# Optimization experiments

Measured on AMD Instinct MI355X. Metric: run time of the kernel, lower is better.

Reference implementation:

```python
import jax, jax.numpy as jnp
import numpy as np
from jax import lax


def setup_inputs() -> dict:
    key = jax.random.key(0)
    k1, k2 = jax.random.split(key)
    x = jax.random.normal(k1, (16, 256, 64, 64), dtype=jnp.float32)
    weight = jax.random.normal(k2, (1024, 256), dtype=jnp.float32)  # codebook (K, C)
    return {"x": x, "weight": weight}


def reference(x, weight):
    B, C, H, W = x.shape
    # (b c h w) -> (b h w) c
    xf = jnp.transpose(x, (0, 2, 3, 1)).reshape(-1, C)  # [N, C]
    d = (jnp.sum(xf * xf, axis=1, keepdims=True)
         + jnp.sum(weight * weight, axis=1)
         - 2.0 * (xf @ weight.T))
    indices = jnp.argmin(d, axis=1)  # [N], int
    z = weight[indices]  # [N, C] embedding lookup
    codebook_loss = jnp.mean((z - lax.stop_gradient(xf)) ** 2)
    commitment_loss = jnp.mean((xf - lax.stop_gradient(z)) ** 2)
    # straight-through estimator
    zq = xf + lax.stop_gradient(z - xf)
    zq = zq.reshape(B, H, W, C).transpose(0, 3, 1, 2)  # back to [B, C, H, W]
    sequence = indices.reshape(B, H, W)
    return zq, sequence, codebook_loss, commitment_loss
```

## Files before the change

### kernel.cpp

```cpp
#include <hip/hip_runtime.h>
#include <cfloat>
#include <climits>

#define B_   16
#define C_   256
#define K_   1024
#define HW_  4096
#define N_   (B_ * HW_)
#define CHW_ (C_ * HW_)

#define SEQ_OFF  16777216
#define LOSS_OFF (SEQ_OFF + N_)
#define WT_F    0
#define WN_F    262144
#define WNU_F   263168
#define WQ_F    264192
#define RLIST_F 395264
#define RCNT_F  526336
#define WMAX_F  526337

#define RL_CAP  131072
#define EPS_GAP 0.1f
#define XSCL    20.0f
#define XINV    0.05f
#define XOVF    6.3f

typedef int i32x4  __attribute__((ext_vector_type(4)));
typedef int i32x16 __attribute__((ext_vector_type(16)));

__device__ __forceinline__ int pack4b(int b0, int b1, int b2, int b3) {
    return (b0 & 0xFF) | ((b1 & 0xFF) << 8) | ((b2 & 0xFF) << 16) | ((b3 & 0xFF) << 24);
}

__global__ __launch_bounds__(256) void wmax_kernel(
    const float* __restrict__ w, unsigned* __restrict__ wmax_bits)
{
    const int tid = blockIdx.x * 256 + threadIdx.x;
    float mx = 0.f;
#pragma unroll
    for (int q = 0; q < 4; ++q) {
        const float4 v = reinterpret_cast<const float4*>(w)[tid * 4 + q];
        mx = fmaxf(mx, fmaxf(fmaxf(fabsf(v.x), fabsf(v.y)), fmaxf(fabsf(v.z), fabsf(v.w))));
    }
#pragma unroll
    for (int m = 1; m < 64; m <<= 1) mx = fmaxf(mx, __shfl_xor(mx, m, 64));
    if ((threadIdx.x & 63) == 0) atomicMax(wmax_bits, __float_as_uint(mx));
}

__global__ __launch_bounds__(256) void wprep_kernel(
    const float* __restrict__ w, const unsigned* __restrict__ wmax_bits,
    unsigned char* __restrict__ wq, float* __restrict__ w_t,
    float* __restrict__ wn, int* __restrict__ wnu)
{
    const int t = threadIdx.x;
    const int l = t & 63;
    const int k = blockIdx.x * 4 + (t >> 6);
    const float wmx = __uint_as_float(*wmax_bits);
    const float s   = 127.4f / wmx;
    const float d1  = wmx / 127.4f;
    const float sl  = s * 256.0f;

    const float4 v4 = *reinterpret_cast<const float4*>(w + (size_t)k * C_ + l * 4);
    float vv[4] = {v4.x, v4.y, v4.z, v4.w};
    float s2 = vv[0]*vv[0] + vv[1]*vv[1] + vv[2]*vv[2] + vv[3]*vv[3];
#pragma unroll
    for (int m = 1; m < 64; m <<= 1) s2 += __shfl_xor(s2, m, 64);

    const int chunk = k >> 5;
    const int col   = k & 31;
#pragma unroll
    for (int q = 0; q < 4; ++q) {
        const int c = l * 4 + q;
        const float v = vv[q];
        const int qh = (int)rintf(v * s);
        const float r = fmaf((float)qh, -d1, v);
        int ql = (int)rintf(r * sl);
        ql = max(-127, min(127, ql));
        const size_t off = (size_t)chunk * 16384 + (size_t)(c >> 5) * 1024
                         + (size_t)((c >> 4) & 1) * 512 + (size_t)col * 16 + (size_t)(c & 15);
        wq[off]        = (unsigned char)(qh & 0xFF);
        wq[off + 8192] = (unsigned char)(ql & 0xFF);
        w_t[(size_t)c * K_ + k] = v;
    }
    if (l == 0) {
        wn[k] = s2;
        wnu[k] = (int)rintf(s2 * (2560.0f / d1));
    }
}

__global__ __launch_bounds__(256) void argmin_i8_kernel(
    const float* __restrict__ x, const unsigned char* __restrict__ wq,
    const int* __restrict__ wnu, const unsigned* __restrict__ wmax_bits,
    float* __restrict__ seq, int* __restrict__ rlist, int* __restrict__ rcount)
{
    __shared__ __align__(16) int   wbuf[2][4096];
    __shared__ __align__(16) float xs[32][128];
    __shared__ int wnu_s[1024];

    const int t  = threadIdx.x;
    const int l  = t & 63;
    const int wv = t >> 6;
    const int col = l & 31;
    const int khalf = l >> 5;
    const int nb = blockIdx.x;
    const int b  = nb >> 5;
    const int hw0 = (nb & 31) << 7;
    const float* xb = x + (size_t)b * CHW_ + hw0;

#define STAGE32(ch, bufidx)                                                       \
    {                                                                             \
        _Pragma("unroll")                                                         \
        for (int rr = 0; rr < 4; ++rr) {                                          \
            const int sIdx = wv * 4 + rr;                                         \
            __builtin_amdgcn_global_load_lds(                                     \
                (const __attribute__((address_space(1))) void*)                   \
                    (wq + (size_t)(ch) * 16384 + sIdx * 1024 + l * 16),           \
                (__attribute__((address_space(3))) void*)                         \
                    (&wbuf[bufidx][sIdx * 256]), 16, 0, 0);                       \
        }                                                                         \
    }

    STAGE32(0, 0);

#pragma unroll
    for (int i = 0; i < 4; ++i) wnu_s[t + i * 256] = wnu[t + i * 256];

    i32x4 ah8[8], al8[8];
    float mx = 0.f;
    {
        const int row = wv * 32 + col;
#pragma unroll
        for (int cc = 0; cc < 8; ++cc) {
#pragma unroll
            for (int qq = 0; qq < 4; ++qq) {
                const int fi = qq * 256 + t;
                const int cl = fi >> 5;
                const int r4 = (fi & 31) << 2;
                const float4 v = *reinterpret_cast<const float4*>(
                    xb + (size_t)(cc * 32 + cl) * HW_ + r4);
                *reinterpret_cast<float4*>(&xs[cl][r4]) = v;
            }
            __syncthreads();
            int qh[16], ql[16];
#pragma unroll
            for (int j = 0; j < 16; ++j) {
                const float v = xs[khalf * 16 + j][row];
                mx = fmaxf(mx, fabsf(v));
                int h = (int)rintf(v * XSCL);
                h = max(-127, min(127, h));
                const float r = fmaf((float)h, -XINV, v);
                int lo = (int)rintf(r * (XSCL * 256.0f));
                lo = max(-127, min(127, lo));
                qh[j] = h; ql[j] = lo;
            }
            ah8[cc] = (i32x4){ pack4b(qh[0],qh[1],qh[2],qh[3]),   pack4b(qh[4],qh[5],qh[6],qh[7]),
                               pack4b(qh[8],qh[9],qh[10],qh[11]), pack4b(qh[12],qh[13],qh[14],qh[15]) };
            al8[cc] = (i32x4){ pack4b(ql[0],ql[1],ql[2],ql[3]),   pack4b(ql[4],ql[5],ql[6],ql[7]),
                               pack4b(ql[8],ql[9],ql[10],ql[11]), pack4b(ql[12],ql[13],ql[14],ql[15]) };
            __syncthreads();
        }
    }

    mx = fmaxf(mx, __shfl_xor(mx, 32, 64));
    if (khalf == 0 && mx > XOVF) {
        const int pos = atomicAdd(rcount, 1);
        if (pos < RL_CAP) rlist[pos] = b * HW_ + hw0 + wv * 32 + col;
    }

    const float wmx = __uint_as_float(*wmax_bits);
    const int eps_u = (int)(32614.4f / wmx);

    int m1p[16], m2p[16];
#pragma unroll
    for (int r = 0; r < 16; ++r) { m1p[r] = INT_MAX; m2p[r] = INT_MAX; }

#pragma unroll 1
    for (int ch = 0; ch < 32; ++ch) {
        const int cur = ch & 1;
        if (ch < 31) STAGE32(ch + 1, cur ^ 1);
        const int wnu_l = wnu_s[ch * 32 + col];

        i32x16 aH, aX;
#pragma unroll
        for (int r = 0; r < 16; ++r) { aH[r] = 0; aX[r] = 0; }

#pragma unroll
        for (int ks = 0; ks < 8; ++ks) {
            const i32x4 bh = *reinterpret_cast<const i32x4*>(&wbuf[cur][ks * 256 + (l << 2)]);
            const i32x4 bl = *reinterpret_cast<const i32x4*>(&wbuf[cur][2048 + ks * 256 + (l << 2)]);
            aH = __builtin_amdgcn_mfma_i32_32x32x32_i8(ah8[ks], bh, aH, 0, 0, 0);
            aX = __builtin_amdgcn_mfma_i32_32x32x32_i8(ah8[ks], bl, aX, 0, 0, 0);
            aX = __builtin_amdgcn_mfma_i32_32x32x32_i8(al8[ks], bh, aX, 0, 0, 0);
        }

#pragma unroll
        for (int r = 0; r < 16; ++r) {
            const int T  = (aH[r] << 8) + aX[r];
            const int D  = wnu_l - T;
            const int Dp = (D & ~31) | ch;
            m2p[r] = min(m2p[r], max(m1p[r], Dp));
            m1p[r] = min(m1p[r], Dp);
        }
        __syncthreads();
    }
#undef STAGE32

    int k1[16];
#pragma unroll
    for (int r = 0; r < 16; ++r) k1[r] = ((m1p[r] & 31) << 5) | col;
#pragma unroll
    for (int mask = 1; mask <= 16; mask <<= 1) {
#pragma unroll
        for (int r = 0; r < 16; ++r) {
            const int om1 = __shfl_xor(m1p[r], mask, 64);
            const int ok1 = __shfl_xor(k1[r],  mask, 64);
            const int om2 = __shfl_xor(m2p[r], mask, 64);
            const int nm2 = min(min(m2p[r], om2), max(m1p[r], om1));
            const bool lt = om1 < m1p[r] || (om1 == m1p[r] && ok1 < k1[r]);
            m1p[r] = lt ? om1 : m1p[r];
            k1[r]  = lt ? ok1 : k1[r];
            m2p[r] = nm2;
        }
    }

    if (col == 0) {
#pragma unroll
        for (int r = 0; r < 16; ++r) {
            const int row_local = (r & 3) + 8 * (r >> 2) + 4 * khalf;
            const int n = b * HW_ + hw0 + wv * 32 + row_local;
            seq[n] = (float)k1[r];
            if (m2p[r] - m1p[r] < eps_u) {
                const int pos = atomicAdd(rcount, 1);
                if (pos < RL_CAP) rlist[pos] = n;
            }
        }
    }
}

__global__ __launch_bounds__(256) void rescue_kernel(
    const float* __restrict__ x, const float* __restrict__ w_t,
    const float* __restrict__ wnorm, const int* __restrict__ rlist,
    const int* __restrict__ rcount, float* __restrict__ seq)
{
    __shared__ float xr[C_];
    __shared__ float bvs[4];
    __shared__ int   bis[4];
    const int t = threadIdx.x;
    const int cnt = min(*rcount, RL_CAP);
    for (int ii = blockIdx.x; ii < cnt; ii += gridDim.x) {
        const int n = rlist[ii];
        const int b = n >> 12, hw = n & 4095;
        xr[t] = x[(size_t)b * CHW_ + (size_t)t * HW_ + hw];
        __syncthreads();
        float best = FLT_MAX; int bidx = 0;
#pragma unroll
        for (int q = 0; q < 4; ++q) {
            const int k = t + q * 256;
            float acc = 0.f;
            for (int c = 0; c < C_; ++c) acc = fmaf(xr[c], w_t[(size_t)c * K_ + k], acc);
            const float d = wnorm[k] - 2.f * acc;
            if (d < best || (d == best && k < bidx)) { best = d; bidx = k; }
        }
#pragma unroll
        for (int mask = 1; mask < 64; mask <<= 1) {
            const float ov = __shfl_xor(best, mask, 64);
            const int   oi = __shfl_xor(bidx, mask, 64);
            if (ov < best || (ov == best && oi < bidx)) { best = ov; bidx = oi; }
        }
        if ((t & 63) == 0) { bvs[t >> 6] = best; bis[t >> 6] = bidx; }
        __syncthreads();
        if (t == 0) {
            float bv = bvs[0]; int bi = bis[0];
#pragma unroll
            for (int w2 = 1; w2 < 4; ++w2)
                if (bvs[w2] < bv || (bvs[w2] == bv && bis[w2] < bi)) { bv = bvs[w2]; bi = bis[w2]; }
            seq[n] = (float)bi;
        }
        __syncthreads();
    }
}

__global__ __launch_bounds__(256) void gather_kernel(
    const float* __restrict__ x, const float* __restrict__ w,
    const float* __restrict__ seqf, float* __restrict__ zq,
    double* __restrict__ loss_acc)
{
    __shared__ float ws[C_ * 64];
    const int t   = threadIdx.x;
    const int nb  = blockIdx.x;
    const int b   = nb >> 6;
    const int hw0 = (nb & 63) << 6;
    {
        const int j = t >> 2, q = t & 3;
        const int idx = (int)seqf[b * HW_ + hw0 + j];
        const float* wrow = w + (size_t)idx * C_ + q * 64;
#pragma unroll
        for (int m = 0; m < 16; ++m) {
            const float4 v = *reinterpret_cast<const float4*>(wrow + m * 4);
            const int c = q * 64 + m * 4;
            ws[(c + 0) * 64 + j] = v.x;
            ws[(c + 1) * 64 + j] = v.y;
            ws[(c + 2) * 64 + j] = v.z;
            ws[(c + 3) * 64 + j] = v.w;
        }
    }
    __syncthreads();
    const int r  = t & 63;
    const int cg = t >> 6;
    const float* xb = x  + (size_t)b * CHW_ + hw0;
    float*       zb = zq + (size_t)b * CHW_ + hw0;
    float lsum = 0.f;
#pragma unroll 4
    for (int cc = 0; cc < 64; ++cc) {
        const int c = cg * 64 + cc;
        const float xv = xb[(size_t)c * HW_ + r];
        const float d  = ws[c * 64 + r] - xv;
        zb[(size_t)c * HW_ + r] = xv + d;
        lsum += d * d;
    }
#pragma unroll
    for (int off = 32; off >= 1; off >>= 1) lsum += __shfl_down(lsum, off, 64);
    __syncthreads();
    if ((t & 63) == 0) ws[t >> 6] = lsum;
    __syncthreads();
    if (t == 0)
        atomicAdd(loss_acc, (double)(ws[0] + ws[1] + ws[2] + ws[3]));
}

__global__ void finalize_kernel(const double* __restrict__ acc, float* __restrict__ loss_out)
{
    const double s = *acc;
    const float m = (float)(s / (double)((size_t)N_ * C_));
    loss_out[0] = m;
    loss_out[1] = m;
}

extern "C" void kernel_launch(void* const* d_in, const int* in_sizes, int n_in,
                              void* d_out, int out_size, void* d_ws, size_t ws_size,
                              hipStream_t stream)
{
    (void)in_sizes; (void)n_in; (void)out_size; (void)d_ws; (void)ws_size;
    const float* x = (const float*)d_in[0];
    const float* w = (const float*)d_in[1];
    float* out = (float*)d_out;

    float*         w_t    = out + WT_F;
    float*         wn     = out + WN_F;
    int*           wnu    = (int*)(out + WNU_F);
    unsigned char* wq     = (unsigned char*)(out + WQ_F);
    int*           rlist  = (int*)(out + RLIST_F);
    int*           rcount = (int*)(out + RCNT_F);
    unsigned*      wmaxb  = (unsigned*)(out + WMAX_F);
    float*         seq    = out + SEQ_OFF;
    double*        loss_acc = (double*)(out + LOSS_OFF);

    hipMemsetAsync((void*)wmaxb, 0, 4, stream);
    hipMemsetAsync((void*)rcount, 0, 4, stream);
    wmax_kernel<<<64, 256, 0, stream>>>(w, wmaxb);
    wprep_kernel<<<256, 256, 0, stream>>>(w, wmaxb, wq, w_t, wn, wnu);
    argmin_i8_kernel<<<512, 256, 0, stream>>>(x, wq, wnu, wmaxb, seq, rlist, rcount);
    rescue_kernel<<<1024, 256, 0, stream>>>(x, w_t, wn, rlist, rcount, seq);
    hipMemsetAsync((char*)d_out + (size_t)LOSS_OFF * 4, 0, 8, stream);
    gather_kernel<<<1024, 256, 0, stream>>>(x, w, seq, out, loss_acc);
    finalize_kernel<<<1, 1, 0, stream>>>(loss_acc, out + LOSS_OFF);
}
```

Before: 201.6 us.

## Alias x staging buffer onto weight LDS and split MFMA accumulators

The 16KB x-staging buffer is removed and the x transpose staging now reuses weight buffer 0, with the first weight chunk prefetched into buffer 1 and the ping-pong order flipped to match. This cuts LDS per block, which may allow more resident blocks per CU. The int8 MFMA chain is also split across four independent accumulators instead of two, which shortens dependent MFMA chains at the cost of extra accumulator registers that could lower occupancy.

```diff
diff --git a/kernel.cpp b/kernel.cpp
--- a/kernel.cpp
+++ b/kernel.cpp
@@ -93,8 +93,7 @@
     const int* __restrict__ wnu, const unsigned* __restrict__ wmax_bits,
     float* __restrict__ seq, int* __restrict__ rlist, int* __restrict__ rcount)
 {
-    __shared__ __align__(16) int   wbuf[2][4096];
-    __shared__ __align__(16) float xs[32][128];
+    __shared__ __align__(16) int wbuf[2][4096];
     __shared__ int wnu_s[1024];
 
     const int t  = threadIdx.x;
@@ -120,7 +119,7 @@
         }                                                                         \
     }
 
-    STAGE32(0, 0);
+    STAGE32(0, 1);
 
 #pragma unroll
     for (int i = 0; i < 4; ++i) wnu_s[t + i * 256] = wnu[t + i * 256];
@@ -128,6 +127,7 @@
     i32x4 ah8[8], al8[8];
     float mx = 0.f;
     {
+        float* xs = reinterpret_cast<float*>(&wbuf[0][0]);
         const int row = wv * 32 + col;
 #pragma unroll
         for (int cc = 0; cc < 8; ++cc) {
@@ -138,13 +138,13 @@
                 const int r4 = (fi & 31) << 2;
                 const float4 v = *reinterpret_cast<const float4*>(
                     xb + (size_t)(cc * 32 + cl) * HW_ + r4);
-                *reinterpret_cast<float4*>(&xs[cl][r4]) = v;
+                *reinterpret_cast<float4*>(&xs[cl * 128 + r4]) = v;
             }
             __syncthreads();
             int qh[16], ql[16];
 #pragma unroll
             for (int j = 0; j < 16; ++j) {
-                const float v = xs[khalf * 16 + j][row];
+                const float v = xs[(khalf * 16 + j) * 128 + row];
                 mx = fmaxf(mx, fabsf(v));
                 int h = (int)rintf(v * XSCL);
                 h = max(-127, min(127, h));
@@ -176,26 +176,31 @@
 
 #pragma unroll 1
     for (int ch = 0; ch < 32; ++ch) {
-        const int cur = ch & 1;
+        const int cur = 1 ^ (ch & 1);
         if (ch < 31) STAGE32(ch + 1, cur ^ 1);
         const int wnu_l = wnu_s[ch * 32 + col];
 
-        i32x16 aH, aX;
-#pragma unroll
-        for (int r = 0; r < 16; ++r) { aH[r] = 0; aX[r] = 0; }
-
-#pragma unroll
-        for (int ks = 0; ks < 8; ++ks) {
-            const i32x4 bh = *reinterpret_cast<const i32x4*>(&wbuf[cur][ks * 256 + (l << 2)]);
-            const i32x4 bl = *reinterpret_cast<const i32x4*>(&wbuf[cur][2048 + ks * 256 + (l << 2)]);
-            aH = __builtin_amdgcn_mfma_i32_32x32x32_i8(ah8[ks], bh, aH, 0, 0, 0);
-            aX = __builtin_amdgcn_mfma_i32_32x32x32_i8(ah8[ks], bl, aX, 0, 0, 0);
-            aX = __builtin_amdgcn_mfma_i32_32x32x32_i8(al8[ks], bh, aX, 0, 0, 0);
+        i32x16 aH1, aH2, aX1, aX2;
+#pragma unroll
+        for (int r = 0; r < 16; ++r) { aH1[r] = 0; aH2[r] = 0; aX1[r] = 0; aX2[r] = 0; }
+
+#pragma unroll
+        for (int ks = 0; ks < 8; ks += 2) {
+            const i32x4 bh0 = *reinterpret_cast<const i32x4*>(&wbuf[cur][ks * 256 + (l << 2)]);
+            const i32x4 bl0 = *reinterpret_cast<const i32x4*>(&wbuf[cur][2048 + ks * 256 + (l << 2)]);
+            const i32x4 bh1 = *reinterpret_cast<const i32x4*>(&wbuf[cur][(ks + 1) * 256 + (l << 2)]);
+            const i32x4 bl1 = *reinterpret_cast<const i32x4*>(&wbuf[cur][2048 + (ks + 1) * 256 + (l << 2)]);
+            aH1 = __builtin_amdgcn_mfma_i32_32x32x32_i8(ah8[ks],     bh0, aH1, 0, 0, 0);
+            aH2 = __builtin_amdgcn_mfma_i32_32x32x32_i8(ah8[ks + 1], bh1, aH2, 0, 0, 0);
+            aX1 = __builtin_amdgcn_mfma_i32_32x32x32_i8(ah8[ks],     bl0, aX1, 0, 0, 0);
+            aX2 = __builtin_amdgcn_mfma_i32_32x32x32_i8(al8[ks],     bh0, aX2, 0, 0, 0);
+            aX1 = __builtin_amdgcn_mfma_i32_32x32x32_i8(ah8[ks + 1], bl1, aX1, 0, 0, 0);
+            aX2 = __builtin_amdgcn_mfma_i32_32x32x32_i8(al8[ks + 1], bh1, aX2, 0, 0, 0);
         }
 
 #pragma unroll
         for (int r = 0; r < 16; ++r) {
-            const int T  = (aH[r] << 8) + aX[r];
+            const int T  = ((aH1[r] + aH2[r]) << 8) + aX1[r] + aX2[r];
             const int D  = wnu_l - T;
             const int Dp = (D & ~31) | ch;
             m2p[r] = min(m2p[r], max(m1p[r], Dp));
```

Result: slower. 208.4 us (+3.3%).

## Drop LDS staging in argmin kernel; one wave per block reading codebook from global

Applied to the files above, without the earlier changes.

Restructures the int8 MFMA argmin kernel from 4-wave blocks that share a double-buffered LDS copy of the quantized codebook to single-wave blocks (2048 blocks of 64 threads). Each wave now loads its B operands straight from global memory into registers, and x is read per lane with strided scalar loads instead of coalesced float4 staging through LDS. This removes LDS traffic and all __syncthreads barriers, relying on L2/L1 for codebook reuse and on more resident waves to hide latency. In exchange, each wave fetches the full codebook itself, raising global and L2 traffic, and the x loads are less coalesced.

```diff
diff --git a/kernel.cpp b/kernel.cpp
--- a/kernel.cpp
+++ b/kernel.cpp
@@ -88,83 +88,45 @@
     }
 }
 
-__global__ __launch_bounds__(256) void argmin_i8_kernel(
+__global__ __launch_bounds__(64, 2) void argmin_i8_kernel(
     const float* __restrict__ x, const unsigned char* __restrict__ wq,
     const int* __restrict__ wnu, const unsigned* __restrict__ wmax_bits,
     float* __restrict__ seq, int* __restrict__ rlist, int* __restrict__ rcount)
 {
-    __shared__ __align__(16) int   wbuf[2][4096];
-    __shared__ __align__(16) float xs[32][128];
-    __shared__ int wnu_s[1024];
-
-    const int t  = threadIdx.x;
-    const int l  = t & 63;
-    const int wv = t >> 6;
+    const int l = threadIdx.x;
     const int col = l & 31;
     const int khalf = l >> 5;
     const int nb = blockIdx.x;
-    const int b  = nb >> 5;
-    const int hw0 = (nb & 31) << 7;
-    const float* xb = x + (size_t)b * CHW_ + hw0;
-
-#define STAGE32(ch, bufidx)                                                       \
-    {                                                                             \
-        _Pragma("unroll")                                                         \
-        for (int rr = 0; rr < 4; ++rr) {                                          \
-            const int sIdx = wv * 4 + rr;                                         \
-            __builtin_amdgcn_global_load_lds(                                     \
-                (const __attribute__((address_space(1))) void*)                   \
-                    (wq + (size_t)(ch) * 16384 + sIdx * 1024 + l * 16),           \
-                (__attribute__((address_space(3))) void*)                         \
-                    (&wbuf[bufidx][sIdx * 256]), 16, 0, 0);                       \
-        }                                                                         \
-    }
-
-    STAGE32(0, 0);
-
-#pragma unroll
-    for (int i = 0; i < 4; ++i) wnu_s[t + i * 256] = wnu[t + i * 256];
+    const int b  = nb >> 7;
+    const int hw0 = (nb & 127) << 5;
+    const float* xb = x + (size_t)b * CHW_ + hw0 + col;
 
     i32x4 ah8[8], al8[8];
     float mx = 0.f;
-    {
-        const int row = wv * 32 + col;
-#pragma unroll
-        for (int cc = 0; cc < 8; ++cc) {
-#pragma unroll
-            for (int qq = 0; qq < 4; ++qq) {
-                const int fi = qq * 256 + t;
-                const int cl = fi >> 5;
-                const int r4 = (fi & 31) << 2;
-                const float4 v = *reinterpret_cast<const float4*>(
-                    xb + (size_t)(cc * 32 + cl) * HW_ + r4);
-                *reinterpret_cast<float4*>(&xs[cl][r4]) = v;
-            }
-            __syncthreads();
-            int qh[16], ql[16];
-#pragma unroll
-            for (int j = 0; j < 16; ++j) {
-                const float v = xs[khalf * 16 + j][row];
-                mx = fmaxf(mx, fabsf(v));
-                int h = (int)rintf(v * XSCL);
-                h = max(-127, min(127, h));
-                const float r = fmaf((float)h, -XINV, v);
-                int lo = (int)rintf(r * (XSCL * 256.0f));
-                lo = max(-127, min(127, lo));
-                qh[j] = h; ql[j] = lo;
-            }
-            ah8[cc] = (i32x4){ pack4b(qh[0],qh[1],qh[2],qh[3]),   pack4b(qh[4],qh[5],qh[6],qh[7]),
-                               pack4b(qh[8],qh[9],qh[10],qh[11]), pack4b(qh[12],qh[13],qh[14],qh[15]) };
-            al8[cc] = (i32x4){ pack4b(ql[0],ql[1],ql[2],ql[3]),   pack4b(ql[4],ql[5],ql[6],ql[7]),
-                               pack4b(ql[8],ql[9],ql[10],ql[11]), pack4b(ql[12],ql[13],ql[14],ql[15]) };
-            __syncthreads();
-        }
+#pragma unroll
+    for (int cc = 0; cc < 8; ++cc) {
+        int qh[16], ql[16];
+#pragma unroll
+        for (int j = 0; j < 16; ++j) {
+            const float v = xb[(size_t)(cc * 32 + khalf * 16 + j) * HW_];
+            mx = fmaxf(mx, fabsf(v));
+            int h = (int)rintf(v * XSCL);
+            h = max(-127, min(127, h));
+            const float r = fmaf((float)h, -XINV, v);
+            int lo = (int)rintf(r * (XSCL * 256.0f));
+            lo = max(-127, min(127, lo));
+            qh[j] = h; ql[j] = lo;
+        }
+        ah8[cc] = (i32x4){ pack4b(qh[0],qh[1],qh[2],qh[3]),   pack4b(qh[4],qh[5],qh[6],qh[7]),
+                           pack4b(qh[8],qh[9],qh[10],qh[11]), pack4b(qh[12],qh[13],qh[14],qh[15]) };
+        al8[cc] = (i32x4){ pack4b(ql[0],ql[1],ql[2],ql[3]),   pack4b(ql[4],ql[5],ql[6],ql[7]),
+                           pack4b(ql[8],ql[9],ql[10],ql[11]), pack4b(ql[12],ql[13],ql[14],ql[15]) };
     }
 
     mx = fmaxf(mx, __shfl_xor(mx, 32, 64));
     if (khalf == 0 && mx > XOVF) {
         const int pos = atomicAdd(rcount, 1);
-        if (pos < RL_CAP) rlist[pos] = b * HW_ + hw0 + wv * 32 + col;
+        if (pos < RL_CAP) rlist[pos] = b * HW_ + hw0 + col;
     }
 
     const float wmx = __uint_as_float(*wmax_bits);
@@ -176,21 +138,29 @@
 
 #pragma unroll 1
     for (int ch = 0; ch < 32; ++ch) {
-        const int cur = ch & 1;
-        if (ch < 31) STAGE32(ch + 1, cur ^ 1);
-        const int wnu_l = wnu_s[ch * 32 + col];
+        const unsigned char* base = wq + (size_t)ch * 16384 + l * 16;
+        const int wnu_l = wnu[ch * 32 + col];
 
         i32x16 aH, aX;
 #pragma unroll
         for (int r = 0; r < 16; ++r) { aH[r] = 0; aX[r] = 0; }
 
 #pragma unroll
-        for (int ks = 0; ks < 8; ++ks) {
-            const i32x4 bh = *reinterpret_cast<const i32x4*>(&wbuf[cur][ks * 256 + (l << 2)]);
-            const i32x4 bl = *reinterpret_cast<const i32x4*>(&wbuf[cur][2048 + ks * 256 + (l << 2)]);
-            aH = __builtin_amdgcn_mfma_i32_32x32x32_i8(ah8[ks], bh, aH, 0, 0, 0);
-            aX = __builtin_amdgcn_mfma_i32_32x32x32_i8(ah8[ks], bl, aX, 0, 0, 0);
-            aX = __builtin_amdgcn_mfma_i32_32x32x32_i8(al8[ks], bh, aX, 0, 0, 0);
+        for (int half = 0; half < 2; ++half) {
+            i32x4 bh[4], bl[4];
+#pragma unroll
+            for (int q = 0; q < 4; ++q) {
+                const int ks = half * 4 + q;
+                bh[q] = *reinterpret_cast<const i32x4*>(base + ks * 1024);
+                bl[q] = *reinterpret_cast<const i32x4*>(base + 8192 + ks * 1024);
+            }
+#pragma unroll
+            for (int q = 0; q < 4; ++q) {
+                const int ks = half * 4 + q;
+                aH = __builtin_amdgcn_mfma_i32_32x32x32_i8(ah8[ks], bh[q], aH, 0, 0, 0);
+                aX = __builtin_amdgcn_mfma_i32_32x32x32_i8(ah8[ks], bl[q], aX, 0, 0, 0);
+                aX = __builtin_amdgcn_mfma_i32_32x32x32_i8(al8[ks], bh[q], aX, 0, 0, 0);
+            }
         }
 
 #pragma unroll
@@ -201,9 +171,7 @@
             m2p[r] = min(m2p[r], max(m1p[r], Dp));
             m1p[r] = min(m1p[r], Dp);
         }
-        __syncthreads();
-    }
-#undef STAGE32
+    }
 
     int k1[16];
 #pragma unroll
@@ -227,7 +195,7 @@
 #pragma unroll
         for (int r = 0; r < 16; ++r) {
             const int row_local = (r & 3) + 8 * (r >> 2) + 4 * khalf;
-            const int n = b * HW_ + hw0 + wv * 32 + row_local;
+            const int n = b * HW_ + hw0 + row_local;
             seq[n] = (float)k1[r];
             if (m2p[r] - m1p[r] < eps_u) {
                 const int pos = atomicAdd(rcount, 1);
@@ -358,7 +326,7 @@
     hipMemsetAsync((void*)rcount, 0, 4, stream);
     wmax_kernel<<<64, 256, 0, stream>>>(w, wmaxb);
     wprep_kernel<<<256, 256, 0, stream>>>(w, wmaxb, wq, w_t, wn, wnu);
-    argmin_i8_kernel<<<512, 256, 0, stream>>>(x, wq, wnu, wmaxb, seq, rlist, rcount);
+    argmin_i8_kernel<<<2048, 64, 0, stream>>>(x, wq, wnu, wmaxb, seq, rlist, rcount);
     rescue_kernel<<<1024, 256, 0, stream>>>(x, w_t, wn, rlist, rcount, seq);
     hipMemsetAsync((char*)d_out + (size_t)LOSS_OFF * 4, 0, 8, stream);
     gather_kernel<<<1024, 256, 0, stream>>>(x, w, seq, out, loss_acc);
```

Result: faster. 193.2 us (-4.2%).
